# Optimization experiments

Measured on AMD Instinct MI355X. Metric: run time of the kernel, lower is better.

Reference implementation:

```python
import math
import jax, jax.numpy as jnp
import numpy as np

KEY_SIZE = 128
VALUE_SIZE = 128


def setup_inputs() -> dict:
    key = jax.random.key(0)
    # channels = value_size + 2*key_size = 384
    x = jax.random.normal(key, (8, VALUE_SIZE + 2 * KEY_SIZE, 32, 32), dtype=jnp.float32)
    return {"x": x}


def _tokens(t):
    # [B, C, H, W] -> [B*H*W, C]  (matches view/transpose/view in torch code)
    B, C = t.shape[0], t.shape[1]
    return t.reshape(B, C, -1).transpose(0, 2, 1).reshape(-1, C)


def reference(x) -> jnp.ndarray:
    B, C, H, W = x.shape
    value = _tokens(x[:, :VALUE_SIZE])                      # [N, V]
    key_t = _tokens(x[:, VALUE_SIZE:VALUE_SIZE + KEY_SIZE])  # [N, K]
    query = _tokens(x[:, VALUE_SIZE + KEY_SIZE:])            # [N, K]
    # Global N x N attention over all batch*spatial positions (faithful to source)
    weight = (query @ key_t.T) / math.sqrt(KEY_SIZE)         # [N, N]
    attention = jax.nn.softmax(weight, axis=1) @ value      # [N, V]
    out = attention.reshape(B, H * W, VALUE_SIZE).transpose(0, 2, 1)
    return out.reshape(B, VALUE_SIZE, H, W)
```

## Files before the change

### kernel.cpp

```cpp
#include <hip/hip_runtime.h>
#include <hip/hip_bf16.h>
#include <stdint.h>

#define N_TOK 8192
#define DDIM  128

typedef _Float16 half2v __attribute__((ext_vector_type(2)));
typedef _Float16 half4v __attribute__((ext_vector_type(4)));
typedef _Float16 half8v __attribute__((ext_vector_type(8)));
typedef float f32x4 __attribute__((ext_vector_type(4)));
typedef half4v half4_ma __attribute__((may_alias));
typedef half8v half8_ma __attribute__((may_alias));
typedef float4 float4_ma __attribute__((may_alias));

#define MFMA16 __builtin_amdgcn_mfma_f32_16x16x16f16
#define MFMA32 __builtin_amdgcn_mfma_f32_16x16x32_f16

#define QSCALE (0.08838834764831845f * 1.4426950408889634f)

__device__ __forceinline__ half2v pkrtz(float a, float b) {
  return __builtin_bit_cast(half2v, __builtin_amdgcn_cvt_pkrtz(a, b));
}

__device__ __forceinline__ void gload_lds16(const _Float16* g, _Float16* l) {
  __builtin_amdgcn_global_load_lds(
      (const __attribute__((address_space(1))) void*)g,
      (__attribute__((address_space(3))) void*)l, 16, 0, 0);
}

__global__ void prep_qk(const float* __restrict__ x,
                        _Float16* __restrict__ Qf, _Float16* __restrict__ Kf) {
  __shared__ float t[32][33];
  const int b   = blockIdx.z >> 1;
  const int isQ = blockIdx.z & 1;
  const int c0  = (isQ ? 256 : 128) + blockIdx.y * 32;
  const int p0  = blockIdx.x * 32;
  const float* src = x + ((size_t)b * 384 + c0) * 1024 + p0;
  t[threadIdx.y][threadIdx.x] = src[threadIdx.y * 1024 + threadIdx.x];
  __syncthreads();
  float v = t[threadIdx.x][threadIdx.y];
  if (isQ) v *= QSCALE;
  _Float16* dst = isQ ? Qf : Kf;
  dst[((size_t)b * 1024 + p0 + threadIdx.y) * DDIM + blockIdx.y * 32 + threadIdx.x] = (_Float16)v;
}

__global__ void prep_v(const float* __restrict__ x, _Float16* __restrict__ Vt) {
  const int i4 = (blockIdx.x * 256 + threadIdx.x) * 4;
  const int v = i4 >> 13, n = i4 & 8191;
  const int b = n >> 10, p = n & 1023;
  const float4 s = *(const float4_ma*)(x + ((size_t)b * 384 + v) * 1024 + p);
  half4v h; h.x = (_Float16)s.x; h.y = (_Float16)s.y; h.z = (_Float16)s.z; h.w = (_Float16)s.w;
  *(half4_ma*)(Vt + (size_t)v * N_TOK + b * 1024 + p) = h;
}

__global__ __launch_bounds__(256, 2) void flash_attn(
    const _Float16* __restrict__ Qf, const _Float16* __restrict__ Kf,
    const _Float16* __restrict__ Vt, _Float16* __restrict__ Opart,
    float* __restrict__ Lsum) {
  __shared__ _Float16 lds[32768];

  const int tid = threadIdx.x;
  const int w = tid >> 6, lane = tid & 63;
  const int quad = lane >> 4, l16 = lane & 15;
  const int ks = blockIdx.y, KS = gridDim.y;
  const int kp = N_TOK / KS;
  const int chunks = kp >> 6;
  const int k0 = ks * kp;
  const int q0 = blockIdx.x * 128;

  half8v qf[2][4];
#pragma unroll
  for (int qt = 0; qt < 2; ++qt) {
    const _Float16* qp = Qf + (size_t)(q0 + w * 32 + qt * 16 + l16) * DDIM + quad * 8;
#pragma unroll
    for (int kb = 0; kb < 4; ++kb) qf[qt][kb] = *(const half8_ma*)(qp + kb * 32);
  }

  f32x4 O[2][8];
#pragma unroll
  for (int qt = 0; qt < 2; ++qt)
#pragma unroll
    for (int vb = 0; vb < 8; ++vb) O[qt][vb] = (f32x4){0.f, 0.f, 0.f, 0.f};
  float ls[2] = {0.f, 0.f};

  const _Float16* srcK[4];
  const _Float16* srcV[4];
  int vslot[4];
#pragma unroll
  for (int j = 0; j < 4; ++j) {
    srcK[j] = Kf + (size_t)(k0 + lane) * DDIM + (w * 4 + j) * 8;
    const int t = (w * 4 + j) * 64 + lane;
    const int v = t >> 3, h = t & 7;
    const int hs = h ^ ((v >> 1) & 7);
    srcV[j] = Vt + (size_t)v * N_TOK + k0 + hs * 8;
    vslot[j] = (w * 4 + j) * 512;
  }

#pragma unroll
  for (int j = 0; j < 4; ++j) {
    gload_lds16(srcK[j], lds + vslot[j]);
    gload_lds16(srcV[j], lds + 8192 + vslot[j]);
  }

  for (int ch = 0; ch < chunks; ++ch) {
    __syncthreads();
    _Float16* buf = lds + (ch & 1) * 16384;
    if (ch + 1 < chunks) {
      _Float16* nbuf = lds + ((ch + 1) & 1) * 16384;
      const int adv = (ch + 1) * 64;
#pragma unroll
      for (int j = 0; j < 4; ++j) {
        gload_lds16(srcK[j] + (size_t)adv * DDIM, nbuf + vslot[j]);
        gload_lds16(srcV[j] + adv, nbuf + 8192 + vslot[j]);
      }
    }
    const _Float16* Ksh = buf;
    const _Float16* Vsh = buf + 8192;

    f32x4 S[2][4];
#pragma unroll
    for (int qt = 0; qt < 2; ++qt)
#pragma unroll
      for (int cb = 0; cb < 4; ++cb) S[qt][cb] = (f32x4){0.f, 0.f, 0.f, 0.f};
#pragma unroll
    for (int kb = 0; kb < 4; ++kb) {
#pragma unroll
      for (int cb = 0; cb < 4; ++cb) {
        half8v kf = *(const half8_ma*)(Ksh + (((kb * 4 + quad) * 64) + cb * 16 + l16) * 8);
        S[0][cb] = MFMA32(kf, qf[0][kb], S[0][cb], 0, 0, 0);
        S[1][cb] = MFMA32(kf, qf[1][kb], S[1][cb], 0, 0, 0);
      }
    }

    half4v P[2][4];
#pragma unroll
    for (int qt = 0; qt < 2; ++qt) {
#pragma unroll
      for (int cb = 0; cb < 4; ++cb) {
        const float p0 = __builtin_amdgcn_exp2f(S[qt][cb][0]);
        const float p1 = __builtin_amdgcn_exp2f(S[qt][cb][1]);
        const float p2 = __builtin_amdgcn_exp2f(S[qt][cb][2]);
        const float p3 = __builtin_amdgcn_exp2f(S[qt][cb][3]);
        ls[qt] += (p0 + p1) + (p2 + p3);
        half2v lo = pkrtz(p0, p1);
        half2v hi = pkrtz(p2, p3);
        P[qt][cb] = __builtin_shufflevector(lo, hi, 0, 1, 2, 3);
      }
    }

#pragma unroll
    for (int cb = 0; cb < 4; ++cb) {
#pragma unroll
      for (int vb = 0; vb < 8; ++vb) {
        const int v = vb * 16 + l16;
        half4v vf = *(const half4_ma*)(Vsh + v * 64 + (((cb * 4 + quad) ^ (l16 & 14)) * 4));
        O[0][vb] = MFMA16(vf, P[0][cb], O[0][vb], 0, 0, 0);
        O[1][vb] = MFMA16(vf, P[1][cb], O[1][vb], 0, 0, 0);
      }
    }
  }

#pragma unroll
  for (int qt = 0; qt < 2; ++qt) {
    ls[qt] += __shfl_xor(ls[qt], 16, 64);
    ls[qt] += __shfl_xor(ls[qt], 32, 64);
  }
  const float rl[2] = {1.f / ls[0], 1.f / ls[1]};
#pragma unroll
  for (int qt = 0; qt < 2; ++qt) {
    const int q = q0 + w * 32 + qt * 16 + l16;
#pragma unroll
    for (int vb = 0; vb < 8; ++vb) {
#pragma unroll
      for (int r = 0; r < 4; ++r) {
        const int v = vb * 16 + quad * 4 + r;
        Opart[((size_t)ks * DDIM + v) * N_TOK + q] = (_Float16)(O[qt][vb][r] * rl[qt]);
      }
    }
  }
  if (lane < 16) {
#pragma unroll
    for (int qt = 0; qt < 2; ++qt)
      Lsum[(size_t)ks * N_TOK + q0 + w * 32 + qt * 16 + lane] = ls[qt];
  }
}

__global__ void combine_kernel(const _Float16* __restrict__ Opart,
                               const float* __restrict__ Lsum,
                               float* __restrict__ out, int KS) {
  const int o = blockIdx.x * 256 + threadIdx.x;
  const int b = o >> 17, v = (o >> 10) & 127, p = o & 1023;
  const int q = (b << 10) | p;
  float num = 0.f, den = 0.f;
  for (int s = 0; s < KS; ++s) {
    const float l = Lsum[(size_t)s * N_TOK + q];
    num += l * (float)Opart[((size_t)s * DDIM + v) * N_TOK + q];
    den += l;
  }
  out[o] = num / den;
}

extern "C" void kernel_launch(void* const* d_in, const int* in_sizes, int n_in,
                              void* d_out, int out_size, void* d_ws, size_t ws_size,
                              hipStream_t stream) {
  const float* x = (const float*)d_in[0];
  float* out = (float*)d_out;
  char* ws = (char*)d_ws;

  const size_t need8 = (6u << 20) + 8 * (2u << 20) + (size_t)8 * N_TOK * 4;
  const int KS = (ws_size >= need8) ? 8 : 4;

  _Float16* Qf    = (_Float16*)(ws);
  _Float16* Kf    = (_Float16*)(ws + (2u << 20));
  _Float16* Vt    = (_Float16*)(ws + (4u << 20));
  _Float16* Opart = (_Float16*)(ws + (6u << 20));
  float*    Lsum  = (float*)(ws + (6u << 20) + (size_t)KS * (2u << 20));

  prep_qk<<<dim3(32, 4, 16), dim3(32, 32), 0, stream>>>(x, Qf, Kf);
  prep_v<<<dim3(1024), dim3(256), 0, stream>>>(x, Vt);
  flash_attn<<<dim3(64, KS), dim3(256), 0, stream>>>(Qf, Kf, Vt, Opart, Lsum);
  combine_kernel<<<dim3(4096), dim3(256), 0, stream>>>(Opart, Lsum, out, KS);
}
```

Before: 118.3 us.

## Double per-block query tile, fuse prep kernels, vectorize combine, use fdot2 row sums

The flash attention kernel now handles 256 queries per block (4 query tiles per wave), so each K/V chunk loaded into LDS is reused by twice as many MFMAs. The launch bound drops to one block per CU to make room for the larger register footprint. The two prep kernels are merged into one launch, the combine kernel processes four outputs per thread with vector loads, and softmax row sums are accumulated with packed fp16 dot2 instructions. The trade-offs are half as many blocks (32xKS), lower occupancy, and row sums taken from fp16-rounded probabilities.

```diff
diff --git a/kernel.cpp b/kernel.cpp
--- a/kernel.cpp
+++ b/kernel.cpp
@@ -4,10 +4,12 @@
 
 #define N_TOK 8192
 #define DDIM  128
+#define QT    4
 
 typedef _Float16 half2v __attribute__((ext_vector_type(2)));
 typedef _Float16 half4v __attribute__((ext_vector_type(4)));
 typedef _Float16 half8v __attribute__((ext_vector_type(8)));
+typedef __fp16  fp16x2 __attribute__((ext_vector_type(2)));
 typedef float f32x4 __attribute__((ext_vector_type(4)));
 typedef half4v half4_ma __attribute__((may_alias));
 typedef half8v half8_ma __attribute__((may_alias));
@@ -22,38 +24,57 @@
   return __builtin_bit_cast(half2v, __builtin_amdgcn_cvt_pkrtz(a, b));
 }
 
+#if __has_builtin(__builtin_amdgcn_fdot2)
+__device__ __forceinline__ float dot2acc(half2v a, float c) {
+  const fp16x2 ones = {(__fp16)1.f, (__fp16)1.f};
+  return __builtin_amdgcn_fdot2(__builtin_bit_cast(fp16x2, a), ones, c, false);
+}
+#else
+__device__ __forceinline__ float dot2acc(half2v a, float c) {
+  return c + (float)a.x + (float)a.y;
+}
+#endif
+
 __device__ __forceinline__ void gload_lds16(const _Float16* g, _Float16* l) {
   __builtin_amdgcn_global_load_lds(
       (const __attribute__((address_space(1))) void*)g,
       (__attribute__((address_space(3))) void*)l, 16, 0, 0);
 }
 
-__global__ void prep_qk(const float* __restrict__ x,
-                        _Float16* __restrict__ Qf, _Float16* __restrict__ Kf) {
+__global__ void prep_all(const float* __restrict__ x,
+                         _Float16* __restrict__ Qf, _Float16* __restrict__ Kf,
+                         _Float16* __restrict__ Vt) {
   __shared__ float t[32][33];
-  const int b   = blockIdx.z >> 1;
-  const int isQ = blockIdx.z & 1;
-  const int c0  = (isQ ? 256 : 128) + blockIdx.y * 32;
-  const int p0  = blockIdx.x * 32;
-  const float* src = x + ((size_t)b * 384 + c0) * 1024 + p0;
-  t[threadIdx.y][threadIdx.x] = src[threadIdx.y * 1024 + threadIdx.x];
-  __syncthreads();
-  float v = t[threadIdx.x][threadIdx.y];
-  if (isQ) v *= QSCALE;
-  _Float16* dst = isQ ? Qf : Kf;
-  dst[((size_t)b * 1024 + p0 + threadIdx.y) * DDIM + blockIdx.y * 32 + threadIdx.x] = (_Float16)v;
-}
-
-__global__ void prep_v(const float* __restrict__ x, _Float16* __restrict__ Vt) {
-  const int i4 = (blockIdx.x * 256 + threadIdx.x) * 4;
-  const int v = i4 >> 13, n = i4 & 8191;
-  const int b = n >> 10, p = n & 1023;
-  const float4 s = *(const float4_ma*)(x + ((size_t)b * 384 + v) * 1024 + p);
-  half4v h; h.x = (_Float16)s.x; h.y = (_Float16)s.y; h.z = (_Float16)s.z; h.w = (_Float16)s.w;
-  *(half4_ma*)(Vt + (size_t)v * N_TOK + b * 1024 + p) = h;
-}
-
-__global__ __launch_bounds__(256, 2) void flash_attn(
+  const int blk = blockIdx.x, tid = threadIdx.x;
+  if (blk < 2048) {
+    const int pt = blk & 31, ct = (blk >> 5) & 3, z = blk >> 7;
+    const int b = z >> 1, isQ = z & 1;
+    const int c0 = (isQ ? 256 : 128) + ct * 32;
+    const int p0 = pt * 32;
+    const int tx = tid & 31, ty0 = tid >> 5;
+    const float* src = x + ((size_t)b * 384 + c0) * 1024 + p0;
+#pragma unroll
+    for (int i = 0; i < 4; ++i)
+      t[ty0 + i * 8][tx] = src[(ty0 + i * 8) * 1024 + tx];
+    __syncthreads();
+    _Float16* dst = isQ ? Qf : Kf;
+    const float sc = isQ ? QSCALE : 1.f;
+#pragma unroll
+    for (int i = 0; i < 4; ++i) {
+      const int ty = ty0 + i * 8;
+      dst[((size_t)b * 1024 + p0 + ty) * DDIM + ct * 32 + tx] = (_Float16)(t[tx][ty] * sc);
+    }
+  } else {
+    const int i4 = ((blk - 2048) * 256 + tid) * 4;
+    const int v = i4 >> 13, n = i4 & 8191;
+    const int b = n >> 10, p = n & 1023;
+    const float4 s = *(const float4_ma*)(x + ((size_t)b * 384 + v) * 1024 + p);
+    half4v h; h.x = (_Float16)s.x; h.y = (_Float16)s.y; h.z = (_Float16)s.z; h.w = (_Float16)s.w;
+    *(half4_ma*)(Vt + (size_t)v * N_TOK + b * 1024 + p) = h;
+  }
+}
+
+__global__ __launch_bounds__(256, 1) void flash_attn(
     const _Float16* __restrict__ Qf, const _Float16* __restrict__ Kf,
     const _Float16* __restrict__ Vt, _Float16* __restrict__ Opart,
     float* __restrict__ Lsum) {
@@ -66,22 +87,22 @@
   const int kp = N_TOK / KS;
   const int chunks = kp >> 6;
   const int k0 = ks * kp;
-  const int q0 = blockIdx.x * 128;
-
-  half8v qf[2][4];
-#pragma unroll
-  for (int qt = 0; qt < 2; ++qt) {
-    const _Float16* qp = Qf + (size_t)(q0 + w * 32 + qt * 16 + l16) * DDIM + quad * 8;
+  const int q0 = blockIdx.x * 256;
+
+  half8v qf[QT][4];
+#pragma unroll
+  for (int qt = 0; qt < QT; ++qt) {
+    const _Float16* qp = Qf + (size_t)(q0 + w * 64 + qt * 16 + l16) * DDIM + quad * 8;
 #pragma unroll
     for (int kb = 0; kb < 4; ++kb) qf[qt][kb] = *(const half8_ma*)(qp + kb * 32);
   }
 
-  f32x4 O[2][8];
-#pragma unroll
-  for (int qt = 0; qt < 2; ++qt)
+  f32x4 O[QT][8];
+#pragma unroll
+  for (int qt = 0; qt < QT; ++qt)
 #pragma unroll
     for (int vb = 0; vb < 8; ++vb) O[qt][vb] = (f32x4){0.f, 0.f, 0.f, 0.f};
-  float ls[2] = {0.f, 0.f};
+  float ls[QT] = {0.f, 0.f, 0.f, 0.f};
 
   const _Float16* srcK[4];
   const _Float16* srcV[4];
@@ -117,9 +138,9 @@
     const _Float16* Ksh = buf;
     const _Float16* Vsh = buf + 8192;
 
-    f32x4 S[2][4];
-#pragma unroll
-    for (int qt = 0; qt < 2; ++qt)
+    f32x4 S[QT][4];
+#pragma unroll
+    for (int qt = 0; qt < QT; ++qt)
 #pragma unroll
       for (int cb = 0; cb < 4; ++cb) S[qt][cb] = (f32x4){0.f, 0.f, 0.f, 0.f};
 #pragma unroll
@@ -127,23 +148,24 @@
 #pragma unroll
       for (int cb = 0; cb < 4; ++cb) {
         half8v kf = *(const half8_ma*)(Ksh + (((kb * 4 + quad) * 64) + cb * 16 + l16) * 8);
-        S[0][cb] = MFMA32(kf, qf[0][kb], S[0][cb], 0, 0, 0);
-        S[1][cb] = MFMA32(kf, qf[1][kb], S[1][cb], 0, 0, 0);
-      }
-    }
-
-    half4v P[2][4];
-#pragma unroll
-    for (int qt = 0; qt < 2; ++qt) {
+#pragma unroll
+        for (int qt = 0; qt < QT; ++qt)
+          S[qt][cb] = MFMA32(kf, qf[qt][kb], S[qt][cb], 0, 0, 0);
+      }
+    }
+
+    half4v P[QT][4];
+#pragma unroll
+    for (int qt = 0; qt < QT; ++qt) {
 #pragma unroll
       for (int cb = 0; cb < 4; ++cb) {
         const float p0 = __builtin_amdgcn_exp2f(S[qt][cb][0]);
         const float p1 = __builtin_amdgcn_exp2f(S[qt][cb][1]);
         const float p2 = __builtin_amdgcn_exp2f(S[qt][cb][2]);
         const float p3 = __builtin_amdgcn_exp2f(S[qt][cb][3]);
-        ls[qt] += (p0 + p1) + (p2 + p3);
         half2v lo = pkrtz(p0, p1);
         half2v hi = pkrtz(p2, p3);
+        ls[qt] = dot2acc(lo, dot2acc(hi, ls[qt]));
         P[qt][cb] = __builtin_shufflevector(lo, hi, 0, 1, 2, 3);
       }
     }
@@ -154,50 +176,55 @@
       for (int vb = 0; vb < 8; ++vb) {
         const int v = vb * 16 + l16;
         half4v vf = *(const half4_ma*)(Vsh + v * 64 + (((cb * 4 + quad) ^ (l16 & 14)) * 4));
-        O[0][vb] = MFMA16(vf, P[0][cb], O[0][vb], 0, 0, 0);
-        O[1][vb] = MFMA16(vf, P[1][cb], O[1][vb], 0, 0, 0);
-      }
-    }
-  }
-
-#pragma unroll
-  for (int qt = 0; qt < 2; ++qt) {
+#pragma unroll
+        for (int qt = 0; qt < QT; ++qt)
+          O[qt][vb] = MFMA16(vf, P[qt][cb], O[qt][vb], 0, 0, 0);
+      }
+    }
+  }
+
+#pragma unroll
+  for (int qt = 0; qt < QT; ++qt) {
     ls[qt] += __shfl_xor(ls[qt], 16, 64);
     ls[qt] += __shfl_xor(ls[qt], 32, 64);
   }
-  const float rl[2] = {1.f / ls[0], 1.f / ls[1]};
-#pragma unroll
-  for (int qt = 0; qt < 2; ++qt) {
-    const int q = q0 + w * 32 + qt * 16 + l16;
+#pragma unroll
+  for (int qt = 0; qt < QT; ++qt) {
+    const float rl = 1.f / ls[qt];
+    const int q = q0 + w * 64 + qt * 16 + l16;
 #pragma unroll
     for (int vb = 0; vb < 8; ++vb) {
 #pragma unroll
       for (int r = 0; r < 4; ++r) {
         const int v = vb * 16 + quad * 4 + r;
-        Opart[((size_t)ks * DDIM + v) * N_TOK + q] = (_Float16)(O[qt][vb][r] * rl[qt]);
+        Opart[((size_t)ks * DDIM + v) * N_TOK + q] = (_Float16)(O[qt][vb][r] * rl);
       }
     }
   }
   if (lane < 16) {
 #pragma unroll
-    for (int qt = 0; qt < 2; ++qt)
-      Lsum[(size_t)ks * N_TOK + q0 + w * 32 + qt * 16 + lane] = ls[qt];
+    for (int qt = 0; qt < QT; ++qt)
+      Lsum[(size_t)ks * N_TOK + q0 + w * 64 + qt * 16 + lane] = ls[qt];
   }
 }
 
 __global__ void combine_kernel(const _Float16* __restrict__ Opart,
                                const float* __restrict__ Lsum,
                                float* __restrict__ out, int KS) {
-  const int o = blockIdx.x * 256 + threadIdx.x;
-  const int b = o >> 17, v = (o >> 10) & 127, p = o & 1023;
+  const int o4 = (blockIdx.x * 256 + threadIdx.x) * 4;
+  const int b = o4 >> 17, v = (o4 >> 10) & 127, p = o4 & 1023;
   const int q = (b << 10) | p;
-  float num = 0.f, den = 0.f;
+  float4 num = make_float4(0.f, 0.f, 0.f, 0.f);
+  float4 den = make_float4(0.f, 0.f, 0.f, 0.f);
   for (int s = 0; s < KS; ++s) {
-    const float l = Lsum[(size_t)s * N_TOK + q];
-    num += l * (float)Opart[((size_t)s * DDIM + v) * N_TOK + q];
-    den += l;
-  }
-  out[o] = num / den;
+    const float4 l = *(const float4_ma*)(Lsum + (size_t)s * N_TOK + q);
+    const half4v ov = *(const half4_ma*)(Opart + ((size_t)s * DDIM + v) * N_TOK + q);
+    num.x += l.x * (float)ov.x; num.y += l.y * (float)ov.y;
+    num.z += l.z * (float)ov.z; num.w += l.w * (float)ov.w;
+    den.x += l.x; den.y += l.y; den.z += l.z; den.w += l.w;
+  }
+  *(float4_ma*)(out + o4) =
+      make_float4(num.x / den.x, num.y / den.y, num.z / den.z, num.w / den.w);
 }
 
 extern "C" void kernel_launch(void* const* d_in, const int* in_sizes, int n_in,
@@ -216,8 +243,7 @@
   _Float16* Opart = (_Float16*)(ws + (6u << 20));
   float*    Lsum  = (float*)(ws + (6u << 20) + (size_t)KS * (2u << 20));
 
-  prep_qk<<<dim3(32, 4, 16), dim3(32, 32), 0, stream>>>(x, Qf, Kf);
-  prep_v<<<dim3(1024), dim3(256), 0, stream>>>(x, Vt);
-  flash_attn<<<dim3(64, KS), dim3(256), 0, stream>>>(Qf, Kf, Vt, Opart, Lsum);
-  combine_kernel<<<dim3(4096), dim3(256), 0, stream>>>(Opart, Lsum, out, KS);
-}
+  prep_all<<<dim3(3072), dim3(256), 0, stream>>>(x, Qf, Kf, Vt);
+  flash_attn<<<dim3(32, KS), dim3(256), 0, stream>>>(Qf, Kf, Vt, Opart, Lsum);
+  combine_kernel<<<dim3(1024), dim3(256), 0, stream>>>(Opart, Lsum, out, KS);
+}
```

Result: slower. 121.3 us (+2.5%).
